# Kernel optimization log

Measured on AMD Instinct MI355X. Metric: run time of the kernel, lower is better.

Reference implementation:

```python
import jax, jax.numpy as jnp
import numpy as np

INPUT_SIZE = 1024
HIDDEN_SIZE = 1024
BATCH = 8192


def setup_inputs() -> dict:
    key = jax.random.key(0)
    ks = jax.random.split(key, 10)
    s_in = 1.0 / np.sqrt(INPUT_SIZE)
    s_h = 1.0 / np.sqrt(HIDDEN_SIZE)
    return {
        "input": jax.random.normal(ks[0], (BATCH, INPUT_SIZE), jnp.float32),
        "hx": jax.random.normal(ks[1], (BATCH, HIDDEN_SIZE), jnp.float32),
        # weights stored [in, out] (transpose of torch Linear)
        "W_ih": jax.random.uniform(ks[2], (INPUT_SIZE, 2 * HIDDEN_SIZE), jnp.float32, -s_in, s_in),
        "b_ih": jax.random.uniform(ks[3], (2 * HIDDEN_SIZE,), jnp.float32, -s_in, s_in),
        "W_hh": jax.random.uniform(ks[4], (HIDDEN_SIZE, 2 * HIDDEN_SIZE), jnp.float32, -s_h, s_h),
        "b_hh": jax.random.uniform(ks[5], (2 * HIDDEN_SIZE,), jnp.float32, -s_h, s_h),
        "W_c": jax.random.uniform(ks[6], (INPUT_SIZE, HIDDEN_SIZE), jnp.float32, -s_in, s_in),
        "b_c": jax.random.uniform(ks[7], (HIDDEN_SIZE,), jnp.float32, -s_in, s_in),
        "W_hc": jax.random.uniform(ks[8], (HIDDEN_SIZE, HIDDEN_SIZE), jnp.float32, -s_h, s_h),
        "b_hc": jax.random.uniform(ks[9], (HIDDEN_SIZE,), jnp.float32, -s_h, s_h),
    }


def reference(input, hx, W_ih, b_ih, W_hh, b_hh, W_c, b_c, W_hc, b_hc):
    H = hx.shape[1]
    gates = jax.nn.sigmoid(input @ W_ih + b_ih + hx @ W_hh + b_hh)  # [B, 2H]
    z_t, r_t = gates[:, :H], gates[:, H:]
    candidate = jnp.tanh(input @ W_c + b_c + r_t * (hx @ W_hc + b_hc))
    return (1.0 - z_t) * hx + z_t * candidate
```

## Files before the change

### kernel.cpp

```cpp
#include <hip/hip_runtime.h>
#include <hip/hip_bf16.h>
#include <cmath>


typedef __attribute__((ext_vector_type(8))) short bf16x8;
typedef __attribute__((ext_vector_type(4))) float f32x4;
typedef unsigned int u32;

typedef const __attribute__((address_space(1))) u32 gu32;
typedef __attribute__((address_space(3))) u32 su32;

__device__ __forceinline__ unsigned short f2bf(float f) {
  union { float f; u32 u; } v; v.f = f;
  u32 u = v.u;
  u += 0x7FFFu + ((u >> 16) & 1u);
  return (unsigned short)(u >> 16);
}

__device__ __forceinline__ void gload16(void* ldsp, const void* gp) {
  __builtin_amdgcn_global_load_lds((gu32*)gp, (su32*)ldsp, 16, 0, 0);
}

__device__ __forceinline__ float sigmf(float x) { return 1.0f / (1.0f + __expf(-x)); }

__global__ __launch_bounds__(256) void cvt_batch_all(
    const float* __restrict__ In, const float* __restrict__ Hx,
    unsigned short* __restrict__ wsIn, unsigned short* __restrict__ wsHx)
{
  int gid = blockIdx.x * 256 + threadIdx.x;
  const float* src; unsigned short* dst; int idx;
  if (gid < (1 << 20)) { src = In; dst = wsIn; idx = gid; }
  else                 { src = Hx; dst = wsHx; idx = gid - (1 << 20); }
  int m = idx >> 7;
  int t = idx & 127;
  const float4* s = (const float4*)(src + (size_t)m * 1024 + t * 8);
  float4 a = s[0], b = s[1];
  int row = m & 127;
  size_t tile = (size_t)(m >> 7) * 32 + (t >> 2);
  int sw = (t & 3) ^ ((row >> 1) & 3);
  bf16x8 v;
  v[0] = (short)f2bf(a.x); v[1] = (short)f2bf(a.y); v[2] = (short)f2bf(a.z); v[3] = (short)f2bf(a.w);
  v[4] = (short)f2bf(b.x); v[5] = (short)f2bf(b.y); v[6] = (short)f2bf(b.z); v[7] = (short)f2bf(b.w);
  *(bf16x8*)(dst + tile * 4096 + row * 32 + sw * 8) = v;
}

__global__ __launch_bounds__(256) void cvt_wt_all(
    const float* __restrict__ Wih, const float* __restrict__ Whh,
    const float* __restrict__ Wc,  const float* __restrict__ Whc,
    unsigned short* __restrict__ wsWih, unsigned short* __restrict__ wsWhh,
    unsigned short* __restrict__ wsWc,  unsigned short* __restrict__ wsWhc)
{
  int bid = blockIdx.x;
  const float* W; unsigned short* dst; int NW; int local;
  if (bid < 1024)      { W = Wih; dst = wsWih; NW = 2048; local = bid; }
  else if (bid < 2048) { W = Whh; dst = wsWhh; NW = 2048; local = bid - 1024; }
  else if (bid < 2560) { W = Wc;  dst = wsWc;  NW = 1024; local = bid - 2048; }
  else                 { W = Whc; dst = wsWhc; NW = 1024; local = bid - 2560; }
  int nb = local >> 5, kb = local & 31;
  int n  = nb * 64 + (threadIdx.x & 63);
  int k0 = kb * 32 + (threadIdx.x >> 6) * 8;
  unsigned short h[8];
  #pragma unroll
  for (int b = 0; b < 8; ++b) h[b] = f2bf(W[(size_t)(k0 + b) * NW + n]);
  int row = n & 63;
  size_t tile = (size_t)(n >> 6) * 32 + (k0 >> 5);
  int sw = ((k0 >> 3) & 3) ^ ((row >> 1) & 3);
  bf16x8 v;
  #pragma unroll
  for (int b = 0; b < 8; ++b) v[b] = (short)h[b];
  *(bf16x8*)(dst + tile * 2048 + row * 32 + sw * 8) = v;
}

__global__ __launch_bounds__(256, 2) void gru_gemm(
    const unsigned short* __restrict__ wsIn, const unsigned short* __restrict__ wsHx,
    const unsigned short* __restrict__ wsWih, const unsigned short* __restrict__ wsWhh,
    const unsigned short* __restrict__ wsWc, const unsigned short* __restrict__ wsWhc,
    const float* __restrict__ Hx,
    const float* __restrict__ bih, const float* __restrict__ bhh,
    const float* __restrict__ bc, const float* __restrict__ bhc,
    float* __restrict__ out)
{
  __shared__ unsigned short lds[20480];
  const int tid  = threadIdx.x;
  const int lane = tid & 63;
  const int wave = tid >> 6;
  const int wm = wave >> 1, wn = wave & 1;
  const int bid = blockIdx.x;
  const int j = bid & 15;
  const int i = bid >> 4;

  const unsigned short* srcB[10];
  int strd[10];
  #pragma unroll
  for (int c0 = 0; c0 < 10; ++c0) {
    int c = wave * 10 + c0;
    const unsigned short* p; int st;
    if (c < 8)       { p = wsIn + (size_t)i * 131072 + c * 512;        st = 4096; }
    else if (c < 16) { p = wsHx + (size_t)i * 131072 + (c - 8) * 512;  st = 4096; }
    else {
      int t = (c - 16) >> 2, cc = (c - 16) & 3;
      const unsigned short* base; int nb;
      if (t == 0)      { base = wsWih; nb = j; }
      else if (t == 1) { base = wsWih; nb = j + 16; }
      else if (t == 2) { base = wsWhh; nb = j; }
      else if (t == 3) { base = wsWhh; nb = j + 16; }
      else if (t == 4) { base = wsWc;  nb = j; }
      else             { base = wsWhc; nb = j; }
      p = base + (size_t)nb * 65536 + cc * 512;
      st = 2048;
    }
    srcB[c0] = p + lane * 8;
    strd[c0] = st;
  }

  f32x4 accZ[4][2], accR[4][2], accC[4][2], accH[4][2];
  #pragma unroll
  for (int a = 0; a < 4; ++a)
    #pragma unroll
    for (int b = 0; b < 2; ++b) {
      accZ[a][b] = (f32x4)(0.0f); accR[a][b] = (f32x4)(0.0f);
      accC[a][b] = (f32x4)(0.0f); accH[a][b] = (f32x4)(0.0f);
    }

  const int r15 = lane & 15;
  const int q   = lane >> 4;

  int aOff[4], wOff[2];
  #pragma unroll
  for (int mr = 0; mr < 4; ++mr) {
    int row = wm * 64 + mr * 16 + r15;
    aOff[mr] = row * 32 + ((q ^ ((row >> 1) & 3)) << 3);
  }
  #pragma unroll
  for (int nr = 0; nr < 2; ++nr) {
    int row = wn * 32 + nr * 16 + r15;
    wOff[nr] = row * 32 + ((q ^ ((row >> 1) & 3)) << 3);
  }

  for (int s = 0; s < 32; ++s) {
    __syncthreads();
    #pragma unroll
    for (int c0 = 0; c0 < 10; ++c0)
      gload16((void*)&lds[(wave * 10 + c0) * 512],
              (const void*)(srcB[c0] + (size_t)s * strd[c0]));
    __syncthreads();

    bf16x8 aIn[4], aHx[4];
    #pragma unroll
    for (int mr = 0; mr < 4; ++mr) {
      aIn[mr] = *(const bf16x8*)&lds[aOff[mr]];
      aHx[mr] = *(const bf16x8*)&lds[4096 + aOff[mr]];
    }
    bf16x8 wf[6][2];
    #pragma unroll
    for (int t = 0; t < 6; ++t)
      #pragma unroll
      for (int nr = 0; nr < 2; ++nr)
        wf[t][nr] = *(const bf16x8*)&lds[8192 + t * 2048 + wOff[nr]];

    #pragma unroll
    for (int mr = 0; mr < 4; ++mr)
      #pragma unroll
      for (int nr = 0; nr < 2; ++nr) {
        accZ[mr][nr] = __builtin_amdgcn_mfma_f32_16x16x32_bf16(aIn[mr], wf[0][nr], accZ[mr][nr], 0, 0, 0);
        accZ[mr][nr] = __builtin_amdgcn_mfma_f32_16x16x32_bf16(aHx[mr], wf[2][nr], accZ[mr][nr], 0, 0, 0);
        accR[mr][nr] = __builtin_amdgcn_mfma_f32_16x16x32_bf16(aIn[mr], wf[1][nr], accR[mr][nr], 0, 0, 0);
        accR[mr][nr] = __builtin_amdgcn_mfma_f32_16x16x32_bf16(aHx[mr], wf[3][nr], accR[mr][nr], 0, 0, 0);
        accC[mr][nr] = __builtin_amdgcn_mfma_f32_16x16x32_bf16(aIn[mr], wf[4][nr], accC[mr][nr], 0, 0, 0);
        accH[mr][nr] = __builtin_amdgcn_mfma_f32_16x16x32_bf16(aHx[mr], wf[5][nr], accH[mr][nr], 0, 0, 0);
      }
  }

  const int n0 = j * 64 + wn * 32;
  const int m0 = i * 128 + wm * 64;
  #pragma unroll
  for (int nr = 0; nr < 2; ++nr) {
    int n = n0 + nr * 16 + r15;
    float bz  = bih[n] + bhh[n];
    float br  = bih[1024 + n] + bhh[1024 + n];
    float bcv = bc[n], bhcv = bhc[n];
    #pragma unroll
    for (int mr = 0; mr < 4; ++mr) {
      #pragma unroll
      for (int v = 0; v < 4; ++v) {
        int m = m0 + mr * 16 + q * 4 + v;
        float z  = sigmf(accZ[mr][nr][v] + bz);
        float rr = sigmf(accR[mr][nr][v] + br);
        float cd = tanhf(accC[mr][nr][v] + bcv + rr * (accH[mr][nr][v] + bhcv));
        float h  = Hx[(size_t)m * 1024 + n];
        out[(size_t)m * 1024 + n] = (1.0f - z) * h + z * cd;
      }
    }
  }
}

__global__ __launch_bounds__(256) void gru_fallback(
    const float* __restrict__ In, const float* __restrict__ Hx,
    const float* __restrict__ Wih, const float* __restrict__ bih,
    const float* __restrict__ Whh, const float* __restrict__ bhh,
    const float* __restrict__ Wc, const float* __restrict__ bc,
    const float* __restrict__ Whc, const float* __restrict__ bhc,
    float* __restrict__ out)
{
  __shared__ float sIn[64][17], sHx[64][17];
  __shared__ float sW[6][16][68];
  const int tid = threadIdx.x;
  const int j = blockIdx.x & 15, i = blockIdx.x >> 4;
  const int tx = tid & 15, ty = tid >> 4;
  float accZ[4][4] = {}, accR[4][4] = {}, accC[4][4] = {}, accH[4][4] = {};
  const int ms = tid >> 2, kq = (tid & 3) * 4;
  const int wk = tid >> 4, wn4 = (tid & 15) * 4;
  for (int k0 = 0; k0 < 1024; k0 += 16) {
    __syncthreads();
    {
      float4 a = *(const float4*)&In[(size_t)(i * 64 + ms) * 1024 + k0 + kq];
      sIn[ms][kq] = a.x; sIn[ms][kq + 1] = a.y; sIn[ms][kq + 2] = a.z; sIn[ms][kq + 3] = a.w;
      float4 b = *(const float4*)&Hx[(size_t)(i * 64 + ms) * 1024 + k0 + kq];
      sHx[ms][kq] = b.x; sHx[ms][kq + 1] = b.y; sHx[ms][kq + 2] = b.z; sHx[ms][kq + 3] = b.w;
    }
    {
      float4 w0 = *(const float4*)&Wih[(size_t)(k0 + wk) * 2048 + j * 64 + wn4];
      float4 w1 = *(const float4*)&Wih[(size_t)(k0 + wk) * 2048 + 1024 + j * 64 + wn4];
      float4 w2 = *(const float4*)&Whh[(size_t)(k0 + wk) * 2048 + j * 64 + wn4];
      float4 w3 = *(const float4*)&Whh[(size_t)(k0 + wk) * 2048 + 1024 + j * 64 + wn4];
      float4 w4 = *(const float4*)&Wc[(size_t)(k0 + wk) * 1024 + j * 64 + wn4];
      float4 w5 = *(const float4*)&Whc[(size_t)(k0 + wk) * 1024 + j * 64 + wn4];
      sW[0][wk][wn4] = w0.x; sW[0][wk][wn4+1] = w0.y; sW[0][wk][wn4+2] = w0.z; sW[0][wk][wn4+3] = w0.w;
      sW[1][wk][wn4] = w1.x; sW[1][wk][wn4+1] = w1.y; sW[1][wk][wn4+2] = w1.z; sW[1][wk][wn4+3] = w1.w;
      sW[2][wk][wn4] = w2.x; sW[2][wk][wn4+1] = w2.y; sW[2][wk][wn4+2] = w2.z; sW[2][wk][wn4+3] = w2.w;
      sW[3][wk][wn4] = w3.x; sW[3][wk][wn4+1] = w3.y; sW[3][wk][wn4+2] = w3.z; sW[3][wk][wn4+3] = w3.w;
      sW[4][wk][wn4] = w4.x; sW[4][wk][wn4+1] = w4.y; sW[4][wk][wn4+2] = w4.z; sW[4][wk][wn4+3] = w4.w;
      sW[5][wk][wn4] = w5.x; sW[5][wk][wn4+1] = w5.y; sW[5][wk][wn4+2] = w5.z; sW[5][wk][wn4+3] = w5.w;
    }
    __syncthreads();
    for (int kk = 0; kk < 16; ++kk) {
      float aI[4], aH[4];
      #pragma unroll
      for (int im = 0; im < 4; ++im) { aI[im] = sIn[ty * 4 + im][kk]; aH[im] = sHx[ty * 4 + im][kk]; }
      #pragma unroll
      for (int jn = 0; jn < 4; ++jn) {
        float w0 = sW[0][kk][tx * 4 + jn], w1 = sW[1][kk][tx * 4 + jn], w2 = sW[2][kk][tx * 4 + jn];
        float w3 = sW[3][kk][tx * 4 + jn], w4 = sW[4][kk][tx * 4 + jn], w5 = sW[5][kk][tx * 4 + jn];
        #pragma unroll
        for (int im = 0; im < 4; ++im) {
          accZ[im][jn] += aI[im] * w0 + aH[im] * w2;
          accR[im][jn] += aI[im] * w1 + aH[im] * w3;
          accC[im][jn] += aI[im] * w4;
          accH[im][jn] += aH[im] * w5;
        }
      }
    }
  }
  #pragma unroll
  for (int jn = 0; jn < 4; ++jn) {
    int n = j * 64 + tx * 4 + jn;
    float bz  = bih[n] + bhh[n];
    float br  = bih[1024 + n] + bhh[1024 + n];
    float bcv = bc[n], bhcv = bhc[n];
    #pragma unroll
    for (int im = 0; im < 4; ++im) {
      int m = i * 64 + ty * 4 + im;
      float z  = sigmf(accZ[im][jn] + bz);
      float rr = sigmf(accR[im][jn] + br);
      float cd = tanhf(accC[im][jn] + bcv + rr * (accH[im][jn] + bhcv));
      float h  = Hx[(size_t)m * 1024 + n];
      out[(size_t)m * 1024 + n] = (1.0f - z) * h + z * cd;
    }
  }
}

extern "C" void kernel_launch(void* const* d_in, const int* in_sizes, int n_in,
                              void* d_out, int out_size, void* d_ws, size_t ws_size,
                              hipStream_t stream) {
  const float* In  = (const float*)d_in[0];
  const float* Hx  = (const float*)d_in[1];
  const float* Wih = (const float*)d_in[2];
  const float* bih = (const float*)d_in[3];
  const float* Whh = (const float*)d_in[4];
  const float* bhh = (const float*)d_in[5];
  const float* Wc  = (const float*)d_in[6];
  const float* bc  = (const float*)d_in[7];
  const float* Whc = (const float*)d_in[8];
  const float* bhc = (const float*)d_in[9];
  float* out = (float*)d_out;

  const size_t WS_NEED = 46137344ull;
  if (ws_size >= WS_NEED) {
    unsigned short* ws    = (unsigned short*)d_ws;
    unsigned short* wsIn  = ws;
    unsigned short* wsHx  = ws + 8388608;
    unsigned short* wsWih = ws + 16777216;
    unsigned short* wsWhh = ws + 18874368;
    unsigned short* wsWc  = ws + 20971520;
    unsigned short* wsWhc = ws + 22020096;
    cvt_batch_all<<<8192, 256, 0, stream>>>(In, Hx, wsIn, wsHx);
    cvt_wt_all<<<3072, 256, 0, stream>>>(Wih, Whh, Wc, Whc, wsWih, wsWhh, wsWc, wsWhc);
    gru_gemm<<<1024, 256, 0, stream>>>(wsIn, wsHx, wsWih, wsWhh, wsWc, wsWhc,
                                       Hx, bih, bhh, bc, bhc, out);
  } else {
    gru_fallback<<<2048, 256, 0, stream>>>(In, Hx, Wih, bih, Whh, bhh, Wc, bc, Whc, bhc, out);
  }
}
```

Baseline: 137.8 us.

## Double-buffer LDS in GRU GEMM and merge conversion kernels into one launch

Result: slower. 161.0 us (+16.8%).

```diff
diff --git a/kernel.cpp b/kernel.cpp
--- a/kernel.cpp
+++ b/kernel.cpp
@@ -23,52 +23,52 @@
 
 __device__ __forceinline__ float sigmf(float x) { return 1.0f / (1.0f + __expf(-x)); }
 
-__global__ __launch_bounds__(256) void cvt_batch_all(
+__global__ __launch_bounds__(256) void cvt_all(
     const float* __restrict__ In, const float* __restrict__ Hx,
-    unsigned short* __restrict__ wsIn, unsigned short* __restrict__ wsHx)
-{
-  int gid = blockIdx.x * 256 + threadIdx.x;
-  const float* src; unsigned short* dst; int idx;
-  if (gid < (1 << 20)) { src = In; dst = wsIn; idx = gid; }
-  else                 { src = Hx; dst = wsHx; idx = gid - (1 << 20); }
-  int m = idx >> 7;
-  int t = idx & 127;
-  const float4* s = (const float4*)(src + (size_t)m * 1024 + t * 8);
-  float4 a = s[0], b = s[1];
-  int row = m & 127;
-  size_t tile = (size_t)(m >> 7) * 32 + (t >> 2);
-  int sw = (t & 3) ^ ((row >> 1) & 3);
-  bf16x8 v;
-  v[0] = (short)f2bf(a.x); v[1] = (short)f2bf(a.y); v[2] = (short)f2bf(a.z); v[3] = (short)f2bf(a.w);
-  v[4] = (short)f2bf(b.x); v[5] = (short)f2bf(b.y); v[6] = (short)f2bf(b.z); v[7] = (short)f2bf(b.w);
-  *(bf16x8*)(dst + tile * 4096 + row * 32 + sw * 8) = v;
-}
-
-__global__ __launch_bounds__(256) void cvt_wt_all(
     const float* __restrict__ Wih, const float* __restrict__ Whh,
     const float* __restrict__ Wc,  const float* __restrict__ Whc,
+    unsigned short* __restrict__ wsIn, unsigned short* __restrict__ wsHx,
     unsigned short* __restrict__ wsWih, unsigned short* __restrict__ wsWhh,
     unsigned short* __restrict__ wsWc,  unsigned short* __restrict__ wsWhc)
 {
   int bid = blockIdx.x;
-  const float* W; unsigned short* dst; int NW; int local;
-  if (bid < 1024)      { W = Wih; dst = wsWih; NW = 2048; local = bid; }
-  else if (bid < 2048) { W = Whh; dst = wsWhh; NW = 2048; local = bid - 1024; }
-  else if (bid < 2560) { W = Wc;  dst = wsWc;  NW = 1024; local = bid - 2048; }
-  else                 { W = Whc; dst = wsWhc; NW = 1024; local = bid - 2560; }
-  int nb = local >> 5, kb = local & 31;
-  int n  = nb * 64 + (threadIdx.x & 63);
-  int k0 = kb * 32 + (threadIdx.x >> 6) * 8;
-  unsigned short h[8];
-  #pragma unroll
-  for (int b = 0; b < 8; ++b) h[b] = f2bf(W[(size_t)(k0 + b) * NW + n]);
-  int row = n & 63;
-  size_t tile = (size_t)(n >> 6) * 32 + (k0 >> 5);
-  int sw = ((k0 >> 3) & 3) ^ ((row >> 1) & 3);
-  bf16x8 v;
-  #pragma unroll
-  for (int b = 0; b < 8; ++b) v[b] = (short)h[b];
-  *(bf16x8*)(dst + tile * 2048 + row * 32 + sw * 8) = v;
+  if (bid < 8192) {
+    int gid = bid * 256 + threadIdx.x;
+    const float* src; unsigned short* dst; int idx;
+    if (gid < (1 << 20)) { src = In; dst = wsIn; idx = gid; }
+    else                 { src = Hx; dst = wsHx; idx = gid - (1 << 20); }
+    int m = idx >> 7;
+    int t = idx & 127;
+    const float4* s = (const float4*)(src + (size_t)m * 1024 + t * 8);
+    float4 a = s[0], b = s[1];
+    int row = m & 127;
+    size_t tile = (size_t)(m >> 7) * 32 + (t >> 2);
+    int sw = (t & 3) ^ ((row >> 1) & 3);
+    bf16x8 v;
+    v[0] = (short)f2bf(a.x); v[1] = (short)f2bf(a.y); v[2] = (short)f2bf(a.z); v[3] = (short)f2bf(a.w);
+    v[4] = (short)f2bf(b.x); v[5] = (short)f2bf(b.y); v[6] = (short)f2bf(b.z); v[7] = (short)f2bf(b.w);
+    *(bf16x8*)(dst + tile * 4096 + row * 32 + sw * 8) = v;
+  } else {
+    int wb = bid - 8192;
+    const float* W; unsigned short* dst; int NW; int local;
+    if (wb < 1024)      { W = Wih; dst = wsWih; NW = 2048; local = wb; }
+    else if (wb < 2048) { W = Whh; dst = wsWhh; NW = 2048; local = wb - 1024; }
+    else if (wb < 2560) { W = Wc;  dst = wsWc;  NW = 1024; local = wb - 2048; }
+    else                { W = Whc; dst = wsWhc; NW = 1024; local = wb - 2560; }
+    int nb = local >> 5, kb = local & 31;
+    int n  = nb * 64 + (threadIdx.x & 63);
+    int k0 = kb * 32 + (threadIdx.x >> 6) * 8;
+    unsigned short h[8];
+    #pragma unroll
+    for (int b = 0; b < 8; ++b) h[b] = f2bf(W[(size_t)(k0 + b) * NW + n]);
+    int row = n & 63;
+    size_t tile = (size_t)(n >> 6) * 32 + (k0 >> 5);
+    int sw = ((k0 >> 3) & 3) ^ ((row >> 1) & 3);
+    bf16x8 v;
+    #pragma unroll
+    for (int b = 0; b < 8; ++b) v[b] = (short)h[b];
+    *(bf16x8*)(dst + tile * 2048 + row * 32 + sw * 8) = v;
+  }
 }
 
 __global__ __launch_bounds__(256, 2) void gru_gemm(
@@ -80,7 +80,7 @@
     const float* __restrict__ bc, const float* __restrict__ bhc,
     float* __restrict__ out)
 {
-  __shared__ unsigned short lds[20480];
+  __shared__ unsigned short lds[40960];
   const int tid  = threadIdx.x;
   const int lane = tid & 63;
   const int wave = tid >> 6;
@@ -112,6 +112,7 @@
     srcB[c0] = p + lane * 8;
     strd[c0] = st;
   }
+  const int stageOff = (wave * 10) * 512;
 
   f32x4 accZ[4][2], accR[4][2], accC[4][2], accH[4][2];
   #pragma unroll
@@ -137,27 +138,28 @@
     wOff[nr] = row * 32 + ((q ^ ((row >> 1) & 3)) << 3);
   }
 
-  for (int s = 0; s < 32; ++s) {
-    __syncthreads();
+  auto stage = [&](int bufBase, int s) {
     #pragma unroll
     for (int c0 = 0; c0 < 10; ++c0)
-      gload16((void*)&lds[(wave * 10 + c0) * 512],
+      gload16((void*)&lds[bufBase + stageOff + c0 * 512],
               (const void*)(srcB[c0] + (size_t)s * strd[c0]));
-    __syncthreads();
-
+  };
+
+  auto compute = [&](const unsigned short* __restrict__ L) {
     bf16x8 aIn[4], aHx[4];
     #pragma unroll
     for (int mr = 0; mr < 4; ++mr) {
-      aIn[mr] = *(const bf16x8*)&lds[aOff[mr]];
-      aHx[mr] = *(const bf16x8*)&lds[4096 + aOff[mr]];
+      aIn[mr] = *(const bf16x8*)&L[aOff[mr]];
+      aHx[mr] = *(const bf16x8*)&L[4096 + aOff[mr]];
     }
     bf16x8 wf[6][2];
     #pragma unroll
     for (int t = 0; t < 6; ++t)
       #pragma unroll
       for (int nr = 0; nr < 2; ++nr)
-        wf[t][nr] = *(const bf16x8*)&lds[8192 + t * 2048 + wOff[nr]];
-
+        wf[t][nr] = *(const bf16x8*)&L[8192 + t * 2048 + wOff[nr]];
+
+    __builtin_amdgcn_s_setprio(1);
     #pragma unroll
     for (int mr = 0; mr < 4; ++mr)
       #pragma unroll
@@ -169,6 +171,23 @@
         accC[mr][nr] = __builtin_amdgcn_mfma_f32_16x16x32_bf16(aIn[mr], wf[4][nr], accC[mr][nr], 0, 0, 0);
         accH[mr][nr] = __builtin_amdgcn_mfma_f32_16x16x32_bf16(aHx[mr], wf[5][nr], accH[mr][nr], 0, 0, 0);
       }
+    __builtin_amdgcn_s_setprio(0);
+  };
+
+  stage(0, 0);
+  __syncthreads();
+
+  #pragma unroll 1
+  for (int it = 0; it < 16; ++it) {
+    const int s = it * 2;
+    stage(20480, s + 1);
+    __builtin_amdgcn_sched_barrier(0);
+    compute(&lds[0]);
+    __syncthreads();
+    if (it < 15) stage(0, s + 2);
+    __builtin_amdgcn_sched_barrier(0);
+    compute(&lds[20480]);
+    __syncthreads();
   }
 
   const int n0 = j * 64 + wn * 32;
@@ -293,8 +312,8 @@
     unsigned short* wsWhh = ws + 18874368;
     unsigned short* wsWc  = ws + 20971520;
     unsigned short* wsWhc = ws + 22020096;
-    cvt_batch_all<<<8192, 256, 0, stream>>>(In, Hx, wsIn, wsHx);
-    cvt_wt_all<<<3072, 256, 0, stream>>>(Wih, Whh, Wc, Whc, wsWih, wsWhh, wsWc, wsWhc);
+    cvt_all<<<11264, 256, 0, stream>>>(In, Hx, Wih, Whh, Wc, Whc,
+                                       wsIn, wsHx, wsWih, wsWhh, wsWc, wsWhc);
     gru_gemm<<<1024, 256, 0, stream>>>(wsIn, wsHx, wsWih, wsWhh, wsWc, wsWhc,
                                        Hx, bih, bhh, bc, bhc, out);
   } else {
```

## Pipeline GRU GEMM with multi-buffered LDS, larger block tile, and fused conversion

Applied to the files above, without the earlier changes.

New measurement: 205.0 us. 48.8% more time.

```diff
diff --git a/kernel.cpp b/kernel.cpp
--- a/kernel.cpp
+++ b/kernel.cpp
@@ -16,102 +16,89 @@
   u += 0x7FFFu + ((u >> 16) & 1u);
   return (unsigned short)(u >> 16);
 }
-
 __device__ __forceinline__ void gload16(void* ldsp, const void* gp) {
   __builtin_amdgcn_global_load_lds((gu32*)gp, (su32*)ldsp, 16, 0, 0);
 }
-
 __device__ __forceinline__ float sigmf(float x) { return 1.0f / (1.0f + __expf(-x)); }
 
-__global__ __launch_bounds__(256) void cvt_batch_all(
+#define SB0   __builtin_amdgcn_sched_barrier(0)
+#define LGKM(N) do { asm volatile("s_waitcnt lgkmcnt(" #N ")" ::: "memory"); SB0; } while (0)
+#define VM0     do { asm volatile("s_waitcnt vmcnt(0)"        ::: "memory"); SB0; } while (0)
+#define VM7     do { asm volatile("s_waitcnt vmcnt(7)"        ::: "memory"); SB0; } while (0)
+#define BARR    do { SB0; __builtin_amdgcn_s_barrier(); SB0; } while (0)
+
+__global__ __launch_bounds__(256) void cvt_all(
     const float* __restrict__ In, const float* __restrict__ Hx,
-    unsigned short* __restrict__ wsIn, unsigned short* __restrict__ wsHx)
-{
-  int gid = blockIdx.x * 256 + threadIdx.x;
-  const float* src; unsigned short* dst; int idx;
-  if (gid < (1 << 20)) { src = In; dst = wsIn; idx = gid; }
-  else                 { src = Hx; dst = wsHx; idx = gid - (1 << 20); }
-  int m = idx >> 7;
-  int t = idx & 127;
-  const float4* s = (const float4*)(src + (size_t)m * 1024 + t * 8);
-  float4 a = s[0], b = s[1];
-  int row = m & 127;
-  size_t tile = (size_t)(m >> 7) * 32 + (t >> 2);
-  int sw = (t & 3) ^ ((row >> 1) & 3);
-  bf16x8 v;
-  v[0] = (short)f2bf(a.x); v[1] = (short)f2bf(a.y); v[2] = (short)f2bf(a.z); v[3] = (short)f2bf(a.w);
-  v[4] = (short)f2bf(b.x); v[5] = (short)f2bf(b.y); v[6] = (short)f2bf(b.z); v[7] = (short)f2bf(b.w);
-  *(bf16x8*)(dst + tile * 4096 + row * 32 + sw * 8) = v;
-}
-
-__global__ __launch_bounds__(256) void cvt_wt_all(
     const float* __restrict__ Wih, const float* __restrict__ Whh,
     const float* __restrict__ Wc,  const float* __restrict__ Whc,
-    unsigned short* __restrict__ wsWih, unsigned short* __restrict__ wsWhh,
-    unsigned short* __restrict__ wsWc,  unsigned short* __restrict__ wsWhc)
+    unsigned short* __restrict__ ws)
 {
+  unsigned short* wsIn = ws;
+  unsigned short* wsHx = ws + 8388608;
+  unsigned short* wsW  = ws + 16777216;
   int bid = blockIdx.x;
-  const float* W; unsigned short* dst; int NW; int local;
-  if (bid < 1024)      { W = Wih; dst = wsWih; NW = 2048; local = bid; }
-  else if (bid < 2048) { W = Whh; dst = wsWhh; NW = 2048; local = bid - 1024; }
-  else if (bid < 2560) { W = Wc;  dst = wsWc;  NW = 1024; local = bid - 2048; }
-  else                 { W = Whc; dst = wsWhc; NW = 1024; local = bid - 2560; }
-  int nb = local >> 5, kb = local & 31;
-  int n  = nb * 64 + (threadIdx.x & 63);
-  int k0 = kb * 32 + (threadIdx.x >> 6) * 8;
-  unsigned short h[8];
-  #pragma unroll
-  for (int b = 0; b < 8; ++b) h[b] = f2bf(W[(size_t)(k0 + b) * NW + n]);
-  int row = n & 63;
-  size_t tile = (size_t)(n >> 6) * 32 + (k0 >> 5);
-  int sw = ((k0 >> 3) & 3) ^ ((row >> 1) & 3);
-  bf16x8 v;
-  #pragma unroll
-  for (int b = 0; b < 8; ++b) v[b] = (short)h[b];
-  *(bf16x8*)(dst + tile * 2048 + row * 32 + sw * 8) = v;
-}
-
-__global__ __launch_bounds__(256, 2) void gru_gemm(
-    const unsigned short* __restrict__ wsIn, const unsigned short* __restrict__ wsHx,
-    const unsigned short* __restrict__ wsWih, const unsigned short* __restrict__ wsWhh,
-    const unsigned short* __restrict__ wsWc, const unsigned short* __restrict__ wsWhc,
+  if (bid < 8192) {
+    int gid = bid * 256 + threadIdx.x;
+    const float* src; unsigned short* dst; int idx;
+    if (gid < (1 << 20)) { src = In; dst = wsIn; idx = gid; }
+    else                 { src = Hx; dst = wsHx; idx = gid - (1 << 20); }
+    int m = idx >> 7, t = idx & 127;
+    const float4* s = (const float4*)(src + (size_t)m * 1024 + t * 8);
+    float4 a = s[0], b = s[1];
+    int row = m & 127;
+    size_t tile = (size_t)(m >> 7) * 32 + (t >> 2);
+    int sw = (t & 3) ^ ((row >> 1) & 3);
+    bf16x8 v;
+    v[0] = (short)f2bf(a.x); v[1] = (short)f2bf(a.y); v[2] = (short)f2bf(a.z); v[3] = (short)f2bf(a.w);
+    v[4] = (short)f2bf(b.x); v[5] = (short)f2bf(b.y); v[6] = (short)f2bf(b.z); v[7] = (short)f2bf(b.w);
+    *(bf16x8*)(dst + tile * 4096 + row * 32 + sw * 8) = v;
+  } else {
+    int wb = bid - 8192;
+    const float* W; int NW, tz, local;
+    if (wb < 1024)      { W = Wih; NW = 2048; tz = 0; local = wb; }
+    else if (wb < 2048) { W = Whh; NW = 2048; tz = 1; local = wb - 1024; }
+    else if (wb < 2560) { W = Wc;  NW = 1024; tz = 4; local = wb - 2048; }
+    else                { W = Whc; NW = 1024; tz = 5; local = wb - 2560; }
+    int nb = local >> 5, kb = local & 31;
+    int jj   = nb & 15;
+    int tile = (tz < 4) ? (nb < 16 ? tz : tz + 2) : tz;
+    int n  = nb * 64 + (threadIdx.x & 63);
+    int k0 = kb * 32 + (threadIdx.x >> 6) * 8;
+    bf16x8 v;
+    #pragma unroll
+    for (int b = 0; b < 8; ++b) v[b] = (short)f2bf(W[(size_t)(k0 + b) * NW + n]);
+    int row = n & 63;
+    int sw  = ((k0 >> 3) & 3) ^ ((row >> 1) & 3);
+    *(bf16x8*)(wsW + (size_t)jj * 393216 + (size_t)kb * 12288 + tile * 2048 + row * 32 + sw * 8) = v;
+  }
+}
+
+__global__ __launch_bounds__(512, 2) void gru_gemm(
+    const unsigned short* __restrict__ ws,
     const float* __restrict__ Hx,
     const float* __restrict__ bih, const float* __restrict__ bhh,
     const float* __restrict__ bc, const float* __restrict__ bhc,
     float* __restrict__ out)
 {
-  __shared__ unsigned short lds[20480];
-  const int tid  = threadIdx.x;
-  const int lane = tid & 63;
-  const int wave = tid >> 6;
+  __shared__ unsigned short lds[69632];
+  const int tid = threadIdx.x, lane = tid & 63, wave = tid >> 6;
   const int wm = wave >> 1, wn = wave & 1;
   const int bid = blockIdx.x;
-  const int j = bid & 15;
-  const int i = bid >> 4;
-
-  const unsigned short* srcB[10];
-  int strd[10];
-  #pragma unroll
-  for (int c0 = 0; c0 < 10; ++c0) {
-    int c = wave * 10 + c0;
-    const unsigned short* p; int st;
-    if (c < 8)       { p = wsIn + (size_t)i * 131072 + c * 512;        st = 4096; }
-    else if (c < 16) { p = wsHx + (size_t)i * 131072 + (c - 8) * 512;  st = 4096; }
-    else {
-      int t = (c - 16) >> 2, cc = (c - 16) & 3;
-      const unsigned short* base; int nb;
-      if (t == 0)      { base = wsWih; nb = j; }
-      else if (t == 1) { base = wsWih; nb = j + 16; }
-      else if (t == 2) { base = wsWhh; nb = j; }
-      else if (t == 3) { base = wsWhh; nb = j + 16; }
-      else if (t == 4) { base = wsWc;  nb = j; }
-      else             { base = wsWhc; nb = j; }
-      p = base + (size_t)nb * 65536 + cc * 512;
-      st = 2048;
-    }
-    srcB[c0] = p + lane * 8;
-    strd[c0] = st;
-  }
+  const int swz = (bid & 7) * 64 + (bid >> 3);
+  const int j = swz & 15, i = swz >> 4;
+  const int r15 = lane & 15, q = lane >> 4;
+  const int slot = q ^ ((r15 >> 1) & 3);
+
+  const int vA  = (wm >> 1) * 4096 + (wm & 1) * 2048 + r15 * 32 + slot * 8;
+  const int vW0 = 32768 + wn * 1024 + r15 * 32 + slot * 8;
+  const int vW1 = vW0 + 12288;
+  const int vW2 = vW0 + 24576;
+
+  const int ac = wave * 4;
+  u32 oA = (ac < 16 ? (u32)(2 * i + (ac >> 3)) * 131072u
+                    : 8388608u + (u32)(2 * i + ((ac >> 3) - 2)) * 131072u)
+           + (u32)(ac & 7) * 512u + (u32)lane * 8u;
+  u32 oW = 16777216u + (u32)j * 393216u + (u32)(wave * 3) * 512u + (u32)lane * 8u;
 
   f32x4 accZ[4][2], accR[4][2], accC[4][2], accH[4][2];
   #pragma unroll
@@ -122,57 +109,87 @@
       accC[a][b] = (f32x4)(0.0f); accH[a][b] = (f32x4)(0.0f);
     }
 
-  const int r15 = lane & 15;
-  const int q   = lane >> 4;
-
-  int aOff[4], wOff[2];
-  #pragma unroll
-  for (int mr = 0; mr < 4; ++mr) {
-    int row = wm * 64 + mr * 16 + r15;
-    aOff[mr] = row * 32 + ((q ^ ((row >> 1) & 3)) << 3);
-  }
-  #pragma unroll
-  for (int nr = 0; nr < 2; ++nr) {
-    int row = wn * 32 + nr * 16 + r15;
-    wOff[nr] = row * 32 + ((q ^ ((row >> 1) & 3)) << 3);
-  }
-
-  for (int s = 0; s < 32; ++s) {
-    __syncthreads();
-    #pragma unroll
-    for (int c0 = 0; c0 < 10; ++c0)
-      gload16((void*)&lds[(wave * 10 + c0) * 512],
-              (const void*)(srcB[c0] + (size_t)s * strd[c0]));
-    __syncthreads();
-
-    bf16x8 aIn[4], aHx[4];
-    #pragma unroll
-    for (int mr = 0; mr < 4; ++mr) {
-      aIn[mr] = *(const bf16x8*)&lds[aOff[mr]];
-      aHx[mr] = *(const bf16x8*)&lds[4096 + aOff[mr]];
-    }
-    bf16x8 wf[6][2];
-    #pragma unroll
-    for (int t = 0; t < 6; ++t)
-      #pragma unroll
-      for (int nr = 0; nr < 2; ++nr)
-        wf[t][nr] = *(const bf16x8*)&lds[8192 + t * 2048 + wOff[nr]];
-
-    #pragma unroll
-    for (int mr = 0; mr < 4; ++mr)
-      #pragma unroll
-      for (int nr = 0; nr < 2; ++nr) {
-        accZ[mr][nr] = __builtin_amdgcn_mfma_f32_16x16x32_bf16(aIn[mr], wf[0][nr], accZ[mr][nr], 0, 0, 0);
-        accZ[mr][nr] = __builtin_amdgcn_mfma_f32_16x16x32_bf16(aHx[mr], wf[2][nr], accZ[mr][nr], 0, 0, 0);
-        accR[mr][nr] = __builtin_amdgcn_mfma_f32_16x16x32_bf16(aIn[mr], wf[1][nr], accR[mr][nr], 0, 0, 0);
-        accR[mr][nr] = __builtin_amdgcn_mfma_f32_16x16x32_bf16(aHx[mr], wf[3][nr], accR[mr][nr], 0, 0, 0);
-        accC[mr][nr] = __builtin_amdgcn_mfma_f32_16x16x32_bf16(aIn[mr], wf[4][nr], accC[mr][nr], 0, 0, 0);
-        accH[mr][nr] = __builtin_amdgcn_mfma_f32_16x16x32_bf16(aHx[mr], wf[5][nr], accH[mr][nr], 0, 0, 0);
-      }
-  }
+  bf16x8 aIn0[4], aHx0[4], aIn1[4], aHx1[4];
+  bf16x8 wzA[2], wzB[2], wrA[2], wrB[2], wcA[2], whB[2];
+
+  #define LA(ACb, SEL, MR) (*(const bf16x8*)&lds[(ACb)*16384 + (SEL)*8192 + (MR)*512 + vA])
+  #define LW(K, T, NR)     (*(const bf16x8*)&lds[vW##K + (T)*2048 + (NR)*512])
+
+  #define STAGE(ACb, WSv) { \
+    _Pragma("unroll") for (int c_ = 0; c_ < 4; ++c_) \
+      gload16((void*)&lds[(ACb)*16384 + (wave*4 + c_)*512], (const void*)(ws + oA + c_*512u)); \
+    _Pragma("unroll") for (int c_ = 0; c_ < 3; ++c_) \
+      gload16((void*)&lds[32768 + (WSv)*12288 + (wave*3 + c_)*512], (const void*)(ws + oW + c_*512u)); \
+  }
+
+  #define MFMA_(a,b,c) __builtin_amdgcn_mfma_f32_16x16x32_bf16(a, b, c, 0, 0, 0)
+  #define MZ(AI, AH) { __builtin_amdgcn_s_setprio(1); \
+    _Pragma("unroll") for (int m_=0;m_<4;++m_) { _Pragma("unroll") for (int n_=0;n_<2;++n_) { \
+      accZ[m_][n_] = MFMA_(AI[m_], wzA[n_], accZ[m_][n_]); \
+      accZ[m_][n_] = MFMA_(AH[m_], wzB[n_], accZ[m_][n_]); } } \
+    __builtin_amdgcn_s_setprio(0); }
+  #define MR_(AI, AH) { __builtin_amdgcn_s_setprio(1); \
+    _Pragma("unroll") for (int m_=0;m_<4;++m_) { _Pragma("unroll") for (int n_=0;n_<2;++n_) { \
+      accR[m_][n_] = MFMA_(AI[m_], wrA[n_], accR[m_][n_]); \
+      accR[m_][n_] = MFMA_(AH[m_], wrB[n_], accR[m_][n_]); } } \
+    __builtin_amdgcn_s_setprio(0); }
+  #define MCH(AI, AH) { __builtin_amdgcn_s_setprio(1); \
+    _Pragma("unroll") for (int m_=0;m_<4;++m_) { _Pragma("unroll") for (int n_=0;n_<2;++n_) { \
+      accC[m_][n_] = MFMA_(AI[m_], wcA[n_], accC[m_][n_]); \
+      accH[m_][n_] = MFMA_(AH[m_], whB[n_], accH[m_][n_]); } } \
+    __builtin_amdgcn_s_setprio(0); }
+
+  #define STEP(ACb, WC_, WN_, WS_, AIC, AHC, AIN, AHN) { \
+     \
+    wrA[0] = LW(WC_,2,0); wrA[1] = LW(WC_,2,1); \
+    wrB[0] = LW(WC_,3,0); wrB[1] = LW(WC_,3,1); \
+    wcA[0] = LW(WC_,4,0); wcA[1] = LW(WC_,4,1); \
+    whB[0] = LW(WC_,5,0); whB[1] = LW(WC_,5,1); \
+    LGKM(8); \
+    MZ(AIC, AHC); \
+    VM0; BARR; \
+     \
+    STAGE(ACb, WS_); \
+    wzA[0] = LW(WN_,0,0); wzA[1] = LW(WN_,0,1); \
+    wzB[0] = LW(WN_,1,0); wzB[1] = LW(WN_,1,1); \
+    LGKM(8); \
+    MR_(AIC, AHC); \
+     \
+    AIN[0] = LA((ACb)^1,0,0); AIN[1] = LA((ACb)^1,0,1); \
+    AIN[2] = LA((ACb)^1,0,2); AIN[3] = LA((ACb)^1,0,3); \
+    AHN[0] = LA((ACb)^1,1,0); AHN[1] = LA((ACb)^1,1,1); \
+    AHN[2] = LA((ACb)^1,1,2); AHN[3] = LA((ACb)^1,1,3); \
+    LGKM(12); \
+    MCH(AIC, AHC); \
+    if (tt < 29) { oA += 4096u; oW += 12288u; } ++tt; \
+  }
+
+  STAGE(0, 0); oA += 4096u; oW += 12288u;
+  STAGE(1, 1); oA += 4096u; oW += 12288u;
+  VM7;
+  BARR;
+  aIn0[0] = LA(0,0,0); aIn0[1] = LA(0,0,1); aIn0[2] = LA(0,0,2); aIn0[3] = LA(0,0,3);
+  aHx0[0] = LA(0,1,0); aHx0[1] = LA(0,1,1); aHx0[2] = LA(0,1,2); aHx0[3] = LA(0,1,3);
+  wzA[0] = LW(0,0,0); wzA[1] = LW(0,0,1);
+  wzB[0] = LW(0,1,0); wzB[1] = LW(0,1,1);
+
+  int tt = 0;
+  #pragma unroll 1
+  for (int it = 0; it < 5; ++it) {
+    STEP(0, 0, 1, 2, aIn0, aHx0, aIn1, aHx1)
+    STEP(1, 1, 2, 0, aIn1, aHx1, aIn0, aHx0)
+    STEP(0, 2, 0, 1, aIn0, aHx0, aIn1, aHx1)
+    STEP(1, 0, 1, 2, aIn1, aHx1, aIn0, aHx0)
+    STEP(0, 1, 2, 0, aIn0, aHx0, aIn1, aHx1)
+    STEP(1, 2, 0, 1, aIn1, aHx1, aIn0, aHx0)
+  }
+  STEP(0, 0, 1, 2, aIn0, aHx0, aIn1, aHx1)
+  STEP(1, 1, 2, 0, aIn1, aHx1, aIn0, aHx0)
+  asm volatile("s_waitcnt vmcnt(0) lgkmcnt(0)" ::: "memory");
+  SB0;
 
   const int n0 = j * 64 + wn * 32;
-  const int m0 = i * 128 + wm * 64;
+  const int m0 = i * 256 + wm * 64;
   #pragma unroll
   for (int nr = 0; nr < 2; ++nr) {
     int n = n0 + nr * 16 + r15;
@@ -192,6 +209,14 @@
       }
     }
   }
+  #undef STEP
+  #undef MCH
+  #undef MR_
+  #undef MZ
+  #undef MFMA_
+  #undef STAGE
+  #undef LW
+  #undef LA
 }
 
 __global__ __launch_bounds__(256) void gru_fallback(
@@ -286,17 +311,9 @@
 
   const size_t WS_NEED = 46137344ull;
   if (ws_size >= WS_NEED) {
-    unsigned short* ws    = (unsigned short*)d_ws;
-    unsigned short* wsIn  = ws;
-    unsigned short* wsHx  = ws + 8388608;
-    unsigned short* wsWih = ws + 16777216;
-    unsigned short* wsWhh = ws + 18874368;
-    unsigned short* wsWc  = ws + 20971520;
-    unsigned short* wsWhc = ws + 22020096;
-    cvt_batch_all<<<8192, 256, 0, stream>>>(In, Hx, wsIn, wsHx);
-    cvt_wt_all<<<3072, 256, 0, stream>>>(Wih, Whh, Wc, Whc, wsWih, wsWhh, wsWc, wsWhc);
-    gru_gemm<<<1024, 256, 0, stream>>>(wsIn, wsHx, wsWih, wsWhh, wsWc, wsWhc,
-                                       Hx, bih, bhh, bc, bhc, out);
+    unsigned short* ws = (unsigned short*)d_ws;
+    cvt_all<<<11264, 256, 0, stream>>>(In, Hx, Wih, Whh, Wc, Whc, ws);
+    gru_gemm<<<512, 512, 0, stream>>>(ws, Hx, bih, bhh, bc, bhc, out);
   } else {
     gru_fallback<<<2048, 256, 0, stream>>>(In, Hx, Wih, bih, Whh, bhh, Wc, bc, Whc, bhc, out);
   }
```
